# Kernel tuning notes

Measured on AMD Instinct MI355X. Metric: run time of the kernel, lower is better.

## Reference

```python
import jax, jax.numpy as jnp
import numpy as np

N_NODES = 50000
N_RELS = 100000
N_TRIPLES = 100000
D = 512          # node_dim == rel_dim
H = 768          # hidden_dim
NUM_LAYERS = 3
B = 16           # number of images (segments)
EPS = 1e-5


def setup_inputs() -> dict:
    key = jax.random.key(0)
    ks = jax.random.split(key, 12)
    node_feats = jax.random.normal(ks[0], (N_NODES, D), dtype=jnp.float32)
    rel_feats = jax.random.normal(ks[1], (N_RELS, D), dtype=jnp.float32)
    subj = jax.random.randint(ks[2], (N_TRIPLES,), 0, N_NODES)
    rel = jax.random.randint(ks[3], (N_TRIPLES,), 0, N_RELS)
    obj = jax.random.randint(ks[4], (N_TRIPLES,), 0, N_NODES)
    triples = jnp.stack([subj, rel, obj], axis=1).astype(jnp.int64)
    obj_to_img = jnp.sort(jax.random.randint(ks[5], (N_NODES,), 0, B))
    obj_to_img = obj_to_img.at[-1].set(B - 1)  # pin batch_size = B (torch uses max+1)
    obj_to_img = obj_to_img.astype(jnp.int64)
    s = 0.02
    params = dict(
        node_in_w=jax.random.normal(ks[6], (H, D), dtype=jnp.float32) * s,
        node_in_b=jnp.zeros((H,), dtype=jnp.float32),
        rel_in_w=jax.random.normal(ks[7], (H, D), dtype=jnp.float32) * s,
        rel_in_b=jnp.zeros((H,), dtype=jnp.float32),
        proj_w=jax.random.normal(ks[8], (NUM_LAYERS, H, 2 * H), dtype=jnp.float32) * s,
        proj_b=jnp.zeros((NUM_LAYERS, H), dtype=jnp.float32),
        ln_node_g=jnp.ones((H,), dtype=jnp.float32),
        ln_node_b=jnp.zeros((H,), dtype=jnp.float32),
        ln_rel_g=jnp.ones((H,), dtype=jnp.float32),
        ln_rel_b=jnp.zeros((H,), dtype=jnp.float32),
    )
    return dict(node_feats=node_feats, rel_feats=rel_feats, triples=triples,
                obj_to_img=obj_to_img, **params)


def _layer_norm(x, g, b):
    mu = jnp.mean(x, axis=-1, keepdims=True)
    var = jnp.var(x, axis=-1, keepdims=True)
    return (x - mu) * jax.lax.rsqrt(var + EPS) * g + b


def reference(node_feats, rel_feats, triples, obj_to_img,
              node_in_w, node_in_b, rel_in_w, rel_in_b,
              proj_w, proj_b, ln_node_g, ln_node_b, ln_rel_g, ln_rel_b):
    subj_idx, rel_idx, obj_idx = triples[:, 0], triples[:, 1], triples[:, 2]

    node_states = node_feats @ node_in_w.T + node_in_b          # (N_nodes, H)
    rel_states = rel_feats @ rel_in_w.T + rel_in_b               # (N_rels, H)

    for l in range(NUM_LAYERS):
        rel_g = rel_states[rel_idx]                              # (T, H)
        msg_s2o = node_states[subj_idx] + rel_g                  # subject -> object
        msg_o2s = node_states[obj_idx] + rel_g                   # object -> subject
        agg = (jax.ops.segment_sum(msg_s2o, obj_idx, num_segments=N_NODES)
               + jax.ops.segment_sum(msg_o2s, subj_idx, num_segments=N_NODES))
        h = jnp.concatenate([node_states, agg], axis=-1)         # (N_nodes, 2H)
        h = h @ proj_w[l].T + proj_b[l]
        h = jax.nn.silu(h)
        node_states = node_states + h                            # residual (dropout=0)

    node_states = _layer_norm(node_states, ln_node_g, ln_node_b)
    rel_states = _layer_norm(rel_states, ln_rel_g, ln_rel_b)

    sums = jax.ops.segment_sum(node_states, obj_to_img, num_segments=B)
    counts = jax.ops.segment_sum(jnp.ones((N_NODES,), node_states.dtype),
                                 obj_to_img, num_segments=B)
    global_states = sums / jnp.clip(counts, 1.0)[:, None]        # (B, H)
    return node_states, global_states
```

## Files before the change

kernel.cpp:

```cpp
#include <hip/hip_runtime.h>
#include <hip/hip_bf16.h>
#include <math.h>

#define N_NODES   50000
#define N_RELS    100000
#define N_TRIPLES 100000
#define D_IN      512
#define H_DIM     768
#define NUM_LAYERS 3
#define B_IMG     16
#define MP        50048

typedef __attribute__((ext_vector_type(8))) short short8;
typedef __attribute__((ext_vector_type(4))) float f32x4;

typedef const __attribute__((address_space(1))) unsigned int glb_u32;
typedef __attribute__((address_space(3))) unsigned int lds_u32;

__device__ inline short f2bf16s(float f){
  union { __hip_bfloat16 h; unsigned short u; } cv;
  cv.h = __float2bfloat16(f);
  return (short)cv.u;
}
__device__ inline float bf2f(unsigned short u){
  union { unsigned u; float f; } c; c.u = ((unsigned)u)<<16; return c.f;
}
__device__ inline uint2 pack4bf(float4 v){
  uint2 r;
  r.x = ((unsigned)(unsigned short)f2bf16s(v.x)) | (((unsigned)(unsigned short)f2bf16s(v.y))<<16);
  r.y = ((unsigned)(unsigned short)f2bf16s(v.z)) | (((unsigned)(unsigned short)f2bf16s(v.w))<<16);
  return r;
}
__device__ inline float4 unpack4bf(uint2 p){
  float4 v;
  v.x = bf2f((unsigned short)(p.x & 0xffff)); v.y = bf2f((unsigned short)(p.x >> 16));
  v.z = bf2f((unsigned short)(p.y & 0xffff)); v.w = bf2f((unsigned short)(p.y >> 16));
  return v;
}

__global__ void detect_idx64_kernel(const unsigned* __restrict__ tr, int* __restrict__ flag){
  if (threadIdx.x == 0 && blockIdx.x == 0){
    unsigned o = 0;
    for (int k = 0; k < 256; k++) o |= tr[2*k + 1];
    flag[0] = (o == 0) ? 1 : 0;
  }
}

__device__ inline void load_triple(const void* tp, int t, int is64, int& s, int& r, int& o){
  if (is64){
    const long long* p = (const long long*)tp;
    s = (int)p[3*t]; r = (int)p[3*t+1]; o = (int)p[3*t+2];
  } else {
    const int* p = (const int*)tp;
    s = p[3*t]; r = p[3*t+1]; o = p[3*t+2];
  }
  s = (s < 0) ? 0 : (s >= N_NODES ? N_NODES-1 : s);
  o = (o < 0) ? 0 : (o >= N_NODES ? N_NODES-1 : o);
  r = (r < 0) ? 0 : (r >= N_RELS  ? N_RELS-1  : r);
}

__device__ inline int idx_at(const void* p, int i, int is64){
  return is64 ? (int)((const long long*)p)[i] : ((const int*)p)[i];
}

__global__ __launch_bounds__(256)
void hist_kernel(const void* __restrict__ tr, const int* __restrict__ flag,
                 int* __restrict__ deg){
  int t = blockIdx.x*256 + threadIdx.x;
  if (t >= N_TRIPLES) return;
  int s, r, o;
  load_triple(tr, t, flag[0], s, r, o);
  atomicAdd(&deg[o], 1);
  atomicAdd(&deg[s], 1);
}

__global__ __launch_bounds__(1024)
void scan_kernel(const int* __restrict__ deg, int* __restrict__ offs,
                 int* __restrict__ cursor, float* __restrict__ cnt){
  __shared__ int partial[1024];
  int tid = threadIdx.x;
  const int per = (N_NODES + 1023)/1024;
  int start = tid*per, end = start+per; if (end > N_NODES) end = N_NODES;
  if (start > N_NODES) start = N_NODES;
  int s = 0;
  for (int i=start; i<end; i++) s += deg[i];
  partial[tid] = s;
  __syncthreads();
  for (int off=1; off<1024; off<<=1){
    int v = (tid >= off) ? partial[tid-off] : 0;
    __syncthreads();
    partial[tid] += v;
    __syncthreads();
  }
  int run = (tid > 0) ? partial[tid-1] : 0;
  for (int i=start; i<end; i++){
    offs[i] = run; cursor[i] = run; cnt[i] = (float)deg[i];
    run += deg[i];
  }
  if (tid == 1023) offs[N_NODES] = run;
}

__global__ __launch_bounds__(256)
void fill_kernel(const void* __restrict__ tr, const int* __restrict__ flag,
                 int* __restrict__ cursor, int* __restrict__ col_node,
                 int* __restrict__ col_rel){
  int t = blockIdx.x*256 + threadIdx.x;
  if (t >= N_TRIPLES) return;
  int s, r, o;
  load_triple(tr, t, flag[0], s, r, o);
  int p1 = atomicAdd(&cursor[o], 1); col_node[p1] = s; col_rel[p1] = r;
  int p2 = atomicAdd(&cursor[s], 1); col_node[p2] = o; col_rel[p2] = r;
}

__global__ __launch_bounds__(256)
void gather_rel_kernel(const int* __restrict__ offs, const int* __restrict__ col_rel,
                       const float* __restrict__ relf, unsigned short* __restrict__ rfa_bf){
  int v = blockIdx.x*4 + (threadIdx.x >> 6);
  int lane = threadIdx.x & 63;
  float4 a0 = {0,0,0,0}, a1 = {0,0,0,0};
  int lo = offs[v], hi = offs[v+1];
  for (int e=lo; e<hi; e++){
    int r = col_rel[e];
    const float* rp = relf + (size_t)r*D_IN + lane*4;
    float4 x0 = *(const float4*)rp;
    float4 x1 = *(const float4*)(rp + 256);
    a0.x+=x0.x; a0.y+=x0.y; a0.z+=x0.z; a0.w+=x0.w;
    a1.x+=x1.x; a1.y+=x1.y; a1.z+=x1.z; a1.w+=x1.w;
  }
  uint2* out = (uint2*)(rfa_bf + (size_t)v*D_IN);
  out[lane]    = pack4bf(a0);
  out[lane+64] = pack4bf(a1);
}

__global__ __launch_bounds__(256)
void gather_node_bf_kernel(const int* __restrict__ offs, const int* __restrict__ col_node,
                           const unsigned short* __restrict__ seed_bf,
                           const unsigned short* __restrict__ node_bf,
                           unsigned short* __restrict__ agg_bf){
  int v = blockIdx.x*4 + (threadIdx.x >> 6);
  int lane = threadIdx.x & 63;
  const uint2* sp = (const uint2*)(seed_bf + (size_t)v*H_DIM);
  float4 a0 = unpack4bf(sp[lane]);
  float4 a1 = unpack4bf(sp[lane+64]);
  float4 a2 = unpack4bf(sp[lane+128]);
  int lo = offs[v], hi = offs[v+1];
  for (int e=lo; e<hi; e++){
    int u = col_node[e];
    const uint2* np = (const uint2*)(node_bf + (size_t)u*H_DIM);
    float4 x0 = unpack4bf(np[lane]);
    float4 x1 = unpack4bf(np[lane+64]);
    float4 x2 = unpack4bf(np[lane+128]);
    a0.x+=x0.x; a0.y+=x0.y; a0.z+=x0.z; a0.w+=x0.w;
    a1.x+=x1.x; a1.y+=x1.y; a1.z+=x1.z; a1.w+=x1.w;
    a2.x+=x2.x; a2.y+=x2.y; a2.z+=x2.z; a2.w+=x2.w;
  }
  uint2* out = (uint2*)(agg_bf + (size_t)v*H_DIM);
  out[lane]     = pack4bf(a0);
  out[lane+64]  = pack4bf(a1);
  out[lane+128] = pack4bf(a2);
}

__global__ __launch_bounds__(256)
void gather_node_kernel(const int* __restrict__ offs, const int* __restrict__ col_node,
                        const unsigned short* __restrict__ seed_bf,
                        const float* __restrict__ node,
                        unsigned short* __restrict__ agg_bf){
  int v = blockIdx.x*4 + (threadIdx.x >> 6);
  int lane = threadIdx.x & 63;
  const uint2* sp = (const uint2*)(seed_bf + (size_t)v*H_DIM);
  float4 a0 = unpack4bf(sp[lane]);
  float4 a1 = unpack4bf(sp[lane+64]);
  float4 a2 = unpack4bf(sp[lane+128]);
  int lo = offs[v], hi = offs[v+1];
  for (int e=lo; e<hi; e++){
    int u = col_node[e];
    const float* np = node + (size_t)u*H_DIM + lane*4;
    float4 x0 = *(const float4*)np;
    float4 x1 = *(const float4*)(np + 256);
    float4 x2 = *(const float4*)(np + 512);
    a0.x+=x0.x; a0.y+=x0.y; a0.z+=x0.z; a0.w+=x0.w;
    a1.x+=x1.x; a1.y+=x1.y; a1.z+=x1.z; a1.w+=x1.w;
    a2.x+=x2.x; a2.y+=x2.y; a2.z+=x2.z; a2.w+=x2.w;
  }
  uint2* out = (uint2*)(agg_bf + (size_t)v*H_DIM);
  out[lane]     = pack4bf(a0);
  out[lane+64]  = pack4bf(a1);
  out[lane+128] = pack4bf(a2);
}

__device__ inline short8 load_cvt8(const float* __restrict__ p, bool valid){
  short8 r;
  if (valid){
    float4 v0 = *(const float4*)(p);
    float4 v1 = *(const float4*)(p+4);
    r[0]=f2bf16s(v0.x); r[1]=f2bf16s(v0.y); r[2]=f2bf16s(v0.z); r[3]=f2bf16s(v0.w);
    r[4]=f2bf16s(v1.x); r[5]=f2bf16s(v1.y); r[6]=f2bf16s(v1.z); r[7]=f2bf16s(v1.w);
  } else {
    r = (short8)0;
  }
  return r;
}

template<int MODE>
__global__ __launch_bounds__(256)
void gemm_lds(const unsigned short* __restrict__ A1,
              const unsigned short* __restrict__ A2,
              const unsigned short* __restrict__ W,
              const float* __restrict__ bias,
              const float* __restrict__ rowscale,
              float* __restrict__ Cf,
              unsigned short* __restrict__ Cbf,
              int M, int K1, int K2)
{
  __shared__ unsigned short As[128*64];
  __shared__ unsigned short Bs[128*64];
  const int lane = threadIdx.x & 63;
  const int wv   = threadIdx.x >> 6;
  const int llo  = lane & 15, lhi = lane >> 4;
  const int wm   = (wv>>1)*64, wn = (wv&1)*64;

  const int nwg  = gridDim.x;
  const int q8   = nwg >> 3, r8 = nwg & 7;
  const int xcd  = blockIdx.x & 7, base = blockIdx.x >> 3;
  const int virt = (xcd < r8 ? xcd*(q8+1) : r8*(q8+1) + (xcd-r8)*q8) + base;
  const int bm   = (virt / 6) * 128;
  const int bn   = (virt % 6) * 128;
  const int KW   = K1 + K2;

  const int srow = lane >> 3;
  const int scol = ((lane & 7) ^ srow) * 8;

  f32x4 acc[4][4];
  #pragma unroll
  for (int i=0;i<4;i++)
    #pragma unroll
    for (int j=0;j<4;j++) acc[i][j] = (f32x4)(0.0f);

  const unsigned short* Wb = W + (size_t)bn*KW;

  for (int k0=0; k0<KW; k0+=64){
    const unsigned short* Asrc; int ak0, astr;
    if (k0 < K1){ Asrc = A1 + (size_t)bm*K1; ak0 = k0;      astr = K1; }
    else        { Asrc = A2 + (size_t)bm*K2; ak0 = k0 - K1; astr = K2; }
    #pragma unroll
    for (int p=0;p<4;p++){
      int c = wv*4 + p;
      int row = c*8 + srow;
      __builtin_amdgcn_global_load_lds(
        (glb_u32*)(Asrc + (size_t)row*astr + ak0 + scol),
        (lds_u32*)(As + c*512), 16, 0, 0);
      __builtin_amdgcn_global_load_lds(
        (glb_u32*)(Wb + (size_t)row*KW + k0 + scol),
        (lds_u32*)(Bs + c*512), 16, 0, 0);
    }
    __syncthreads();
    #pragma unroll
    for (int kk=0; kk<64; kk+=32){
      short8 a[4], b[4];
      #pragma unroll
      for (int i=0;i<4;i++){
        int rowA = wm + i*16 + llo;
        int rowB = wn + i*16 + llo;
        int c16  = lhi + (kk>>3);
        a[i] = *(const short8*)(As + rowA*64 + ((c16 ^ (rowA&7))*8));
        b[i] = *(const short8*)(Bs + rowB*64 + ((c16 ^ (rowB&7))*8));
      }
      #pragma unroll
      for (int i=0;i<4;i++)
        #pragma unroll
        for (int j=0;j<4;j++)
          acc[i][j] = __builtin_amdgcn_mfma_f32_16x16x32_bf16(a[i], b[j], acc[i][j], 0,0,0);
    }
    __syncthreads();
  }

  #pragma unroll
  for (int j=0;j<4;j++){
    int col = bn + wn + j*16 + llo;
    float bv = bias ? bias[col] : 0.0f;
    #pragma unroll
    for (int i=0;i<4;i++){
      #pragma unroll
      for (int r=0;r<4;r++){
        int row = bm + wm + i*16 + lhi*4 + r;
        if (row < M){
          size_t idx = (size_t)row*H_DIM + col;
          float v = acc[i][j][r];
          if (MODE==0){
            v += bv;
            Cf[idx] = v;
            Cbf[idx] = (unsigned short)f2bf16s(v);
          } else if (MODE==2){
            v += rowscale[row]*bv;
            Cbf[idx] = (unsigned short)f2bf16s(v);
          } else {
            v += bv;
            float s = v / (1.0f + __expf(-v));
            float nv = Cf[idx] + s;
            Cf[idx] = nv;
            Cbf[idx] = (unsigned short)f2bf16s(nv);
          }
        }
      }
    }
  }
}

template<int MODE, int ABF>
__global__ __launch_bounds__(256)
void gemm_in(const float* __restrict__ Xf, const unsigned short* __restrict__ Xbf,
             const unsigned short* __restrict__ W,
             const float* __restrict__ bias, const float* __restrict__ rowscale,
             float* __restrict__ Cf, unsigned short* __restrict__ Cbf,
             int M, int Ka)
{
  const int lane = threadIdx.x & 63;
  const int wv   = threadIdx.x >> 6;
  const int llo  = lane & 15, lhi = lane >> 4;
  const int bm   = blockIdx.x*128 + (wv>>1)*64;
  const int bn   = blockIdx.y*128 + (wv&1)*64;

  f32x4 acc[4][4];
  #pragma unroll
  for (int i=0;i<4;i++)
    #pragma unroll
    for (int j=0;j<4;j++) acc[i][j] = (f32x4)(0.0f);

  for (int k0=0;k0<Ka;k0+=32){
    short8 a[4], b[4];
    #pragma unroll
    for (int i=0;i<4;i++){
      int row = bm + i*16 + llo;
      if (ABF) a[i] = (row < M) ? *(const short8*)(Xbf + (size_t)row*Ka + k0 + lhi*8) : (short8)0;
      else     a[i] = load_cvt8(Xf + (size_t)row*Ka + k0 + lhi*8, row < M);
      b[i] = *(const short8*)(W + (size_t)(bn + i*16 + llo)*Ka + k0 + lhi*8);
    }
    #pragma unroll
    for (int i=0;i<4;i++)
      #pragma unroll
      for (int j=0;j<4;j++)
        acc[i][j] = __builtin_amdgcn_mfma_f32_16x16x32_bf16(a[i], b[j], acc[i][j], 0,0,0);
  }

  #pragma unroll
  for (int j=0;j<4;j++){
    int col = bn + j*16 + llo;
    float bv = bias ? bias[col] : 0.0f;
    #pragma unroll
    for (int i=0;i<4;i++){
      #pragma unroll
      for (int r=0;r<4;r++){
        int row = bm + i*16 + lhi*4 + r;
        if (row < M){
          size_t idx = (size_t)row*H_DIM + col;
          float v = acc[i][j][r];
          if (MODE==2){
            v += rowscale[row]*bv;
            Cbf[idx] = (unsigned short)f2bf16s(v);
          } else {
            Cf[idx] = v + bv;
          }
        }
      }
    }
  }
}

__global__ __launch_bounds__(512)
void gemm_layer(float* __restrict__ node,
                const unsigned short* __restrict__ agg_bf,
                const unsigned short* __restrict__ W,
                const float* __restrict__ bias,
                int M)
{
  const int lane = threadIdx.x & 63;
  const int wv   = threadIdx.x >> 6;
  const int llo  = lane & 15, lhi = lane >> 4;
  const int bm   = blockIdx.x*64;
  const int bn   = wv*96;

  f32x4 acc[4][6];
  #pragma unroll
  for (int i=0;i<4;i++)
    #pragma unroll
    for (int j=0;j<6;j++) acc[i][j] = (f32x4)(0.0f);

  for (int k0=0;k0<H_DIM;k0+=32){
    short8 a[4], b[6];
    #pragma unroll
    for (int i=0;i<4;i++){
      int row = bm + i*16 + llo;
      a[i] = load_cvt8(node + (size_t)row*H_DIM + k0 + lhi*8, row < M);
    }
    #pragma unroll
    for (int j=0;j<6;j++)
      b[j] = *(const short8*)(W + (size_t)(bn + j*16 + llo)*(2*H_DIM) + k0 + lhi*8);
    #pragma unroll
    for (int i=0;i<4;i++)
      #pragma unroll
      for (int j=0;j<6;j++)
        acc[i][j] = __builtin_amdgcn_mfma_f32_16x16x32_bf16(a[i], b[j], acc[i][j], 0,0,0);
  }
  for (int k0=0;k0<H_DIM;k0+=32){
    short8 a[4], b[6];
    #pragma unroll
    for (int i=0;i<4;i++){
      int row = bm + i*16 + llo;
      a[i] = (row < M) ? *(const short8*)(agg_bf + (size_t)row*H_DIM + k0 + lhi*8) : (short8)0;
    }
    #pragma unroll
    for (int j=0;j<6;j++)
      b[j] = *(const short8*)(W + (size_t)(bn + j*16 + llo)*(2*H_DIM) + H_DIM + k0 + lhi*8);
    #pragma unroll
    for (int i=0;i<4;i++)
      #pragma unroll
      for (int j=0;j<6;j++)
        acc[i][j] = __builtin_amdgcn_mfma_f32_16x16x32_bf16(a[i], b[j], acc[i][j], 0,0,0);
  }

  __syncthreads();

  #pragma unroll
  for (int j=0;j<6;j++){
    int col = bn + j*16 + llo;
    float bv = bias[col];
    #pragma unroll
    for (int i=0;i<4;i++){
      #pragma unroll
      for (int r=0;r<4;r++){
        int row = bm + i*16 + lhi*4 + r;
        if (row < M){
          size_t idx = (size_t)row*H_DIM + col;
          float v = acc[i][j][r] + bv;
          float s = v / (1.0f + __expf(-v));
          node[idx] += s;
        }
      }
    }
  }
}

__global__ __launch_bounds__(256)
void cast_bf16_kernel(const float* __restrict__ src, unsigned short* __restrict__ dst,
                      long n){
  long i = ((long)blockIdx.x*blockDim.x + threadIdx.x)*8;
  long stride = (long)gridDim.x*blockDim.x*8;
  for (; i < n; i += stride){
    float4 v0 = *(const float4*)(src+i);
    float4 v1 = *(const float4*)(src+i+4);
    short8 o;
    o[0]=f2bf16s(v0.x); o[1]=f2bf16s(v0.y); o[2]=f2bf16s(v0.z); o[3]=f2bf16s(v0.w);
    o[4]=f2bf16s(v1.x); o[5]=f2bf16s(v1.y); o[6]=f2bf16s(v1.z); o[7]=f2bf16s(v1.w);
    *(short8*)(dst+i) = o;
  }
}

__global__ __launch_bounds__(256)
void ln_kernel(const float* __restrict__ x, const float* __restrict__ g,
               const float* __restrict__ b, float* __restrict__ out){
  int row = blockIdx.x;
  int t = threadIdx.x;
  const float* xr = x + (size_t)row*H_DIM;
  float v0 = xr[t], v1 = xr[t+256], v2 = xr[t+512];
  float s  = v0+v1+v2;
  float ss = v0*v0+v1*v1+v2*v2;
  for (int off=32; off>0; off>>=1){
    s  += __shfl_down(s,  off);
    ss += __shfl_down(ss, off);
  }
  __shared__ float rs_[4], rss_[4];
  __shared__ float mu_s, rstd_s;
  int lane = t & 63, wv = t >> 6;
  if (lane==0){ rs_[wv]=s; rss_[wv]=ss; }
  __syncthreads();
  if (t==0){
    float S  = rs_[0]+rs_[1]+rs_[2]+rs_[3];
    float SS = rss_[0]+rss_[1]+rss_[2]+rss_[3];
    float mu = S * (1.0f/768.0f);
    float var = SS * (1.0f/768.0f) - mu*mu;
    mu_s = mu; rstd_s = rsqrtf(var + 1e-5f);
  }
  __syncthreads();
  float mu = mu_s, rstd = rstd_s;
  float* orow = out + (size_t)row*H_DIM;
  orow[t]     = (v0-mu)*rstd*g[t]     + b[t];
  orow[t+256] = (v1-mu)*rstd*g[t+256] + b[t+256];
  orow[t+512] = (v2-mu)*rstd*g[t+512] + b[t+512];
}

__global__ __launch_bounds__(256)
void pool1_kernel(const float* __restrict__ ln, const void* __restrict__ o2i,
                  const int* __restrict__ flag, float* __restrict__ acc){
  const int ROWS = 125;
  int is64 = flag[0];
  int r0 = blockIdx.x*ROWS;
  int t = threadIdx.x;
  float a0=0.f, a1=0.f, a2=0.f;
  int cur = idx_at(o2i, r0, is64);
  cur = (cur < 0) ? 0 : (cur >= B_IMG ? B_IMG-1 : cur);
  for (int r=r0; r<r0+ROWS; r++){
    int img = idx_at(o2i, r, is64);
    img = (img < 0) ? 0 : (img >= B_IMG ? B_IMG-1 : img);
    if (img != cur){
      atomicAdd(&acc[cur*H_DIM + t],       a0);
      atomicAdd(&acc[cur*H_DIM + t + 256], a1);
      atomicAdd(&acc[cur*H_DIM + t + 512], a2);
      a0 = a1 = a2 = 0.f;
      cur = img;
    }
    const float* xr = ln + (size_t)r*H_DIM;
    a0 += xr[t]; a1 += xr[t+256]; a2 += xr[t+512];
  }
  atomicAdd(&acc[cur*H_DIM + t],       a0);
  atomicAdd(&acc[cur*H_DIM + t + 256], a1);
  atomicAdd(&acc[cur*H_DIM + t + 512], a2);
}

__device__ inline int lbound_idx(const void* a, int n, int v, int is64){
  int lo=0, hi=n;
  while (lo<hi){ int m=(lo+hi)>>1; if (idx_at(a,m,is64) < v) lo=m+1; else hi=m; }
  return lo;
}

__global__ __launch_bounds__(256)
void pool2_kernel(const float* __restrict__ acc, const void* __restrict__ o2i,
                  const int* __restrict__ flag, float* __restrict__ gout){
  int is64 = flag[0];
  int img = blockIdx.x;
  int t = threadIdx.x;
  int lo = lbound_idx(o2i, N_NODES, img,   is64);
  int hi = lbound_idx(o2i, N_NODES, img+1, is64);
  float c = (float)(hi-lo);
  if (c < 1.0f) c = 1.0f;
  float inv = 1.0f / c;
  gout[(size_t)img*H_DIM + t]       = acc[img*H_DIM + t]       * inv;
  gout[(size_t)img*H_DIM + t + 256] = acc[img*H_DIM + t + 256] * inv;
  gout[(size_t)img*H_DIM + t + 512] = acc[img*H_DIM + t + 512] * inv;
}

extern "C" void kernel_launch(void* const* d_in, const int* in_sizes, int n_in,
                              void* d_out, int out_size, void* d_ws, size_t ws_size,
                              hipStream_t stream){
  const float* node_feats = (const float*)d_in[0];
  const float* rel_feats  = (const float*)d_in[1];
  const void*  triples    = d_in[2];
  const void*  o2i        = d_in[3];
  const float* node_in_w  = (const float*)d_in[4];
  const float* node_in_b  = (const float*)d_in[5];
  const float* rel_in_w   = (const float*)d_in[6];
  const float* rel_in_b   = (const float*)d_in[7];
  const float* proj_w     = (const float*)d_in[8];
  const float* proj_b     = (const float*)d_in[9];
  const float* ln_g       = (const float*)d_in[10];
  const float* ln_b       = (const float*)d_in[11];

  float* out_nodes  = (float*)d_out;
  float* out_global = (float*)d_out + (size_t)N_NODES*H_DIM;

  const int  tri_blocks = (N_TRIPLES + 255)/256;
  const int  gat_blocks = N_NODES/4;

  size_t off = 0;
  auto alloc = [&](size_t bytes)->void*{
    void* r = (char*)d_ws + off; off += (bytes + 255) & ~(size_t)255; return r;
  };
  unsigned short* w_node     = (unsigned short*)alloc((size_t)H_DIM*D_IN*2);
  unsigned short* w_rel      = (unsigned short*)alloc((size_t)H_DIM*D_IN*2);
  unsigned short* w_proj     = (unsigned short*)alloc((size_t)NUM_LAYERS*H_DIM*2*H_DIM*2);
  unsigned short* rel_agg_bf = (unsigned short*)alloc((size_t)N_NODES*H_DIM*2);
  unsigned short* shr_bf     = (unsigned short*)alloc((size_t)MP*D_IN*2);
  unsigned short* node_bf0   = (unsigned short*)alloc((size_t)MP*H_DIM*2);
  unsigned short* node_bf1   = (unsigned short*)alloc((size_t)MP*H_DIM*2);
  unsigned short* agg_bf     = (unsigned short*)alloc((size_t)MP*H_DIM*2);
  float*          cnt        = (float*)alloc((size_t)N_NODES*4);
  int*            deg        = (int*)alloc((size_t)N_NODES*4);
  int*            offs       = (int*)alloc((size_t)(N_NODES+1)*4);
  int*            cursor     = (int*)alloc((size_t)N_NODES*4);
  int*            col_node   = (int*)alloc((size_t)2*N_TRIPLES*4);
  int*            col_rel    = (int*)alloc((size_t)2*N_TRIPLES*4);
  int*            flag       = (int*)alloc(256);
  float*          pool_acc   = (float*)alloc((size_t)B_IMG*H_DIM*4);
  size_t need_full = off;

  detect_idx64_kernel<<<1,64,0,stream>>>((const unsigned*)triples, flag);
  hipMemsetAsync(deg, 0, (size_t)N_NODES*4, stream);
  hist_kernel<<<tri_blocks,256,0,stream>>>(triples, flag, deg);
  scan_kernel<<<1,1024,0,stream>>>(deg, offs, cursor, cnt);
  fill_kernel<<<tri_blocks,256,0,stream>>>(triples, flag, cursor, col_node, col_rel);
  cast_bf16_kernel<<<512,256,0,stream>>>(node_in_w, w_node, (long)H_DIM*D_IN);
  cast_bf16_kernel<<<512,256,0,stream>>>(rel_in_w,  w_rel,  (long)H_DIM*D_IN);
  cast_bf16_kernel<<<2048,256,0,stream>>>(proj_w, w_proj, (long)NUM_LAYERS*H_DIM*2*H_DIM);

  if (ws_size >= need_full){
    const int gg = (MP/128) * (H_DIM/128);

    cast_bf16_kernel<<<2048,256,0,stream>>>(node_feats, shr_bf, (long)N_NODES*D_IN);
    gemm_lds<0><<<gg,256,0,stream>>>(shr_bf, nullptr, w_node, node_in_b, nullptr,
                                     out_nodes, node_bf0, N_NODES, D_IN, 0);

    gather_rel_kernel<<<gat_blocks,256,0,stream>>>(offs, col_rel, rel_feats, shr_bf);
    gemm_lds<2><<<gg,256,0,stream>>>(shr_bf, nullptr, w_rel, rel_in_b, cnt,
                                     nullptr, rel_agg_bf, N_NODES, D_IN, 0);

    unsigned short* cur = node_bf0;
    unsigned short* nxt = node_bf1;
    for (int l=0; l<NUM_LAYERS; ++l){
      gather_node_bf_kernel<<<gat_blocks,256,0,stream>>>(offs, col_node, rel_agg_bf,
                                                         cur, agg_bf);
      gemm_lds<1><<<gg,256,0,stream>>>(cur, agg_bf,
                                       w_proj + (size_t)l*H_DIM*2*H_DIM,
                                       proj_b + (size_t)l*H_DIM, nullptr,
                                       out_nodes, nxt, N_NODES, H_DIM, H_DIM);
      unsigned short* t = cur; cur = nxt; nxt = t;
    }
  } else {
    size_t off2 = 0;
    auto alloc2 = [&](size_t bytes)->void*{
      void* r = (char*)d_ws + off2; off2 += (bytes + 255) & ~(size_t)255; return r;
    };
    unsigned short* w_node2  = (unsigned short*)alloc2((size_t)H_DIM*D_IN*2);
    unsigned short* w_rel2   = (unsigned short*)alloc2((size_t)H_DIM*D_IN*2);
    unsigned short* w_proj2  = (unsigned short*)alloc2((size_t)NUM_LAYERS*H_DIM*2*H_DIM*2);
    unsigned short* relagg2  = (unsigned short*)alloc2((size_t)N_NODES*H_DIM*2);
    unsigned short* rfa2     = (unsigned short*)alloc2((size_t)N_NODES*D_IN*2);
    unsigned short* agg2     = (unsigned short*)alloc2((size_t)N_NODES*H_DIM*2);
    float* cnt2   = (float*)alloc2((size_t)N_NODES*4);
    int*   deg2   = (int*)alloc2((size_t)N_NODES*4);
    int*   offs2  = (int*)alloc2((size_t)(N_NODES+1)*4);
    int*   cur2   = (int*)alloc2((size_t)N_NODES*4);
    int*   coln2  = (int*)alloc2((size_t)2*N_TRIPLES*4);
    int*   colr2  = (int*)alloc2((size_t)2*N_TRIPLES*4);
    int*   flag2  = (int*)alloc2(256);
    float* pacc2  = (float*)alloc2((size_t)B_IMG*H_DIM*4);
    if (ws_size < off2) return;

    detect_idx64_kernel<<<1,64,0,stream>>>((const unsigned*)triples, flag2);
    hipMemsetAsync(deg2, 0, (size_t)N_NODES*4, stream);
    hist_kernel<<<tri_blocks,256,0,stream>>>(triples, flag2, deg2);
    scan_kernel<<<1,1024,0,stream>>>(deg2, offs2, cur2, cnt2);
    fill_kernel<<<tri_blocks,256,0,stream>>>(triples, flag2, cur2, coln2, colr2);
    cast_bf16_kernel<<<512,256,0,stream>>>(node_in_w, w_node2, (long)H_DIM*D_IN);
    cast_bf16_kernel<<<512,256,0,stream>>>(rel_in_w,  w_rel2,  (long)H_DIM*D_IN);
    cast_bf16_kernel<<<2048,256,0,stream>>>(proj_w, w_proj2, (long)NUM_LAYERS*H_DIM*2*H_DIM);

    const dim3 gemm_grid((N_NODES + 127)/128, H_DIM/128);
    gemm_in<0,0><<<gemm_grid,256,0,stream>>>(node_feats, nullptr, w_node2, node_in_b, nullptr,
                                             out_nodes, nullptr, N_NODES, D_IN);
    gather_rel_kernel<<<gat_blocks,256,0,stream>>>(offs2, colr2, rel_feats, rfa2);
    gemm_in<2,1><<<gemm_grid,256,0,stream>>>(nullptr, rfa2, w_rel2, rel_in_b, cnt2,
                                             nullptr, relagg2, N_NODES, D_IN);
    for (int l=0; l<NUM_LAYERS; ++l){
      gather_node_kernel<<<gat_blocks,256,0,stream>>>(offs2, coln2, relagg2,
                                                      out_nodes, agg2);
      gemm_layer<<<(N_NODES+63)/64,512,0,stream>>>(out_nodes, agg2,
                                                   w_proj2 + (size_t)l*H_DIM*2*H_DIM,
                                                   proj_b + (size_t)l*H_DIM, N_NODES);
    }
    flag = flag2; pool_acc = pacc2;
  }

  ln_kernel<<<N_NODES,256,0,stream>>>(out_nodes, ln_g, ln_b, out_nodes);
  hipMemsetAsync(pool_acc, 0, (size_t)B_IMG*H_DIM*4, stream);
  pool1_kernel<<<400,256,0,stream>>>(out_nodes, o2i, flag, pool_acc);
  pool2_kernel<<<B_IMG,256,0,stream>>>(pool_acc, o2i, flag, out_global);
}
```

Baseline: 1.811 ms.

## Double-buffer LDS tiles in bf16 GEMM to overlap loads with MFMA

The GEMM kernel's shared-memory A/B tiles are split into two ping-pong buffers. The global-to-LDS load of the next K tile is issued before computing on the current one, so memory latency can hide behind MFMA work. There is one barrier per tile instead of two. LDS use per block doubles, which can lower occupancy, and the unrolled loop assumes an even tile count.

```diff
diff --git a/kernel.cpp b/kernel.cpp
--- a/kernel.cpp
+++ b/kernel.cpp
@@ -212,8 +212,10 @@
               unsigned short* __restrict__ Cbf,
               int M, int K1, int K2)
 {
-  __shared__ unsigned short As[128*64];
-  __shared__ unsigned short Bs[128*64];
+  __shared__ unsigned short As0[128*64];
+  __shared__ unsigned short Bs0[128*64];
+  __shared__ unsigned short As1[128*64];
+  __shared__ unsigned short Bs1[128*64];
   const int lane = threadIdx.x & 63;
   const int wv   = threadIdx.x >> 6;
   const int llo  = lane & 15, lhi = lane >> 4;
@@ -238,41 +240,55 @@
 
   const unsigned short* Wb = W + (size_t)bn*KW;
 
-  for (int k0=0; k0<KW; k0+=64){
-    const unsigned short* Asrc; int ak0, astr;
-    if (k0 < K1){ Asrc = A1 + (size_t)bm*K1; ak0 = k0;      astr = K1; }
-    else        { Asrc = A2 + (size_t)bm*K2; ak0 = k0 - K1; astr = K2; }
-    #pragma unroll
-    for (int p=0;p<4;p++){
-      int c = wv*4 + p;
-      int row = c*8 + srow;
-      __builtin_amdgcn_global_load_lds(
-        (glb_u32*)(Asrc + (size_t)row*astr + ak0 + scol),
-        (lds_u32*)(As + c*512), 16, 0, 0);
-      __builtin_amdgcn_global_load_lds(
-        (glb_u32*)(Wb + (size_t)row*KW + k0 + scol),
-        (lds_u32*)(Bs + c*512), 16, 0, 0);
-    }
+#define STAGE(AS, BS, K0) do{ \
+    int k0_ = (K0); \
+    const unsigned short* Asrc_; int ak0_, astr_; \
+    if (k0_ < K1){ Asrc_ = A1 + (size_t)bm*K1; ak0_ = k0_;      astr_ = K1; } \
+    else         { Asrc_ = A2 + (size_t)bm*K2; ak0_ = k0_ - K1; astr_ = K2; } \
+    _Pragma("unroll") \
+    for (int p_=0;p_<4;p_++){ \
+      int c_ = wv*4 + p_; \
+      int row_ = c_*8 + srow; \
+      __builtin_amdgcn_global_load_lds( \
+        (glb_u32*)(Asrc_ + (size_t)row_*astr_ + ak0_ + scol), \
+        (lds_u32*)(AS + c_*512), 16, 0, 0); \
+      __builtin_amdgcn_global_load_lds( \
+        (glb_u32*)(Wb + (size_t)row_*KW + k0_ + scol), \
+        (lds_u32*)(BS + c_*512), 16, 0, 0); \
+    } }while(0)
+
+#define COMPUTE(AS, BS) do{ \
+    _Pragma("unroll") \
+    for (int kk=0; kk<64; kk+=32){ \
+      short8 a_[4], b_[4]; \
+      _Pragma("unroll") \
+      for (int i=0;i<4;i++){ \
+        int rowA_ = wm + i*16 + llo; \
+        int rowB_ = wn + i*16 + llo; \
+        int c16_  = lhi + (kk>>3); \
+        a_[i] = *(const short8*)(AS + rowA_*64 + ((c16_ ^ (rowA_&7))*8)); \
+        b_[i] = *(const short8*)(BS + rowB_*64 + ((c16_ ^ (rowB_&7))*8)); \
+      } \
+      _Pragma("unroll") \
+      for (int i=0;i<4;i++) \
+        _Pragma("unroll") \
+        for (int j=0;j<4;j++) \
+          acc[i][j] = __builtin_amdgcn_mfma_f32_16x16x32_bf16(a_[i], b_[j], acc[i][j], 0,0,0); \
+    } }while(0)
+
+  const int nt = KW/64;
+  STAGE(As0, Bs0, 0);
+  __syncthreads();
+  for (int kt=0; kt<nt; kt+=2){
+    if (kt+1 < nt) STAGE(As1, Bs1, (kt+1)*64);
+    COMPUTE(As0, Bs0);
     __syncthreads();
-    #pragma unroll
-    for (int kk=0; kk<64; kk+=32){
-      short8 a[4], b[4];
-      #pragma unroll
-      for (int i=0;i<4;i++){
-        int rowA = wm + i*16 + llo;
-        int rowB = wn + i*16 + llo;
-        int c16  = lhi + (kk>>3);
-        a[i] = *(const short8*)(As + rowA*64 + ((c16 ^ (rowA&7))*8));
-        b[i] = *(const short8*)(Bs + rowB*64 + ((c16 ^ (rowB&7))*8));
-      }
-      #pragma unroll
-      for (int i=0;i<4;i++)
-        #pragma unroll
-        for (int j=0;j<4;j++)
-          acc[i][j] = __builtin_amdgcn_mfma_f32_16x16x32_bf16(a[i], b[j], acc[i][j], 0,0,0);
-    }
+    if (kt+2 < nt) STAGE(As0, Bs0, (kt+2)*64);
+    COMPUTE(As1, Bs1);
     __syncthreads();
   }
+#undef STAGE
+#undef COMPUTE
 
   #pragma unroll
   for (int j=0;j<4;j++){
```

After: 1.835 ms. About the same (+1.4%).
